# Optimization experiments

Hardware: AMD Instinct MI355X
Metric: run time of the kernel (lower is better)

## Reference

```python
import jax, jax.numpy as jnp
import numpy as np

E, H, KV, D = 2048, 32, 8, 64  # embed_dim, n_head, n_kv_head, head_dim
B, C = 1, 2048
G = H // KV  # GQA group size = 4


def setup_inputs() -> dict:
    key = jax.random.key(0)
    k0, k1, k2, k3, k4 = jax.random.split(key, 5)
    s = 0.02
    return {
        "x": jax.random.normal(k0, (B, C, E), dtype=jnp.float32),
        "W_q": jax.random.normal(k1, (H * D, E), dtype=jnp.float32) * s,
        "W_k": jax.random.normal(k2, (KV * D, E), dtype=jnp.float32) * s,
        "W_v": jax.random.normal(k3, (KV * D, E), dtype=jnp.float32) * s,
        "W_o": jax.random.normal(k4, (E, H * D), dtype=jnp.float32) * s,
    }


def reference(x, W_q, W_k, W_v, W_o):
    b, c, e = x.shape
    # bias-free projections (nn.Linear applies x @ W.T)
    Q = (x @ W_q.T).reshape(b, c, KV, G, D)   # [B,C,KV,G,D]
    K = (x @ W_k.T).reshape(b, c, KV, D)      # [B,C,KV,D]
    V = (x @ W_v.T).reshape(b, c, KV, D)
    scale = 1.0 / jnp.sqrt(jnp.float32(D))
    # grouped-query attention scores: query heads grouped per KV head
    scores = jnp.einsum("bqkgd,bskd->bkgqs", Q, K) * scale  # [B,KV,G,Cq,Cs]
    causal = jnp.tril(jnp.ones((c, c), dtype=bool))
    scores = jnp.where(causal, scores, jnp.finfo(scores.dtype).min)
    attn = jax.nn.softmax(scores, axis=-1)
    hidden = jnp.einsum("bkgqs,bskd->bqkgd", attn, V)  # [B,Cq,KV,G,D]
    hidden = hidden.reshape(b, c, H * D)
    return hidden @ W_o.T
```

## Files before the change

kernel.cpp:

```cpp
#include <hip/hip_runtime.h>
#include <stdint.h>
#include <stddef.h>

#define CLEN 2048
#define EMB  2048
#define NH   32
#define NKV  8
#define HD   64

#define SZ_X  (CLEN * EMB)
#define SZ_WQ (NH * HD * EMB)
#define SZ_WK (NKV * HD * EMB)
#define SZ_WV (NKV * HD * EMB)
#define SZ_WO (EMB * NH * HD)
#define SZ_ALL (SZ_X + SZ_WQ + SZ_WK + SZ_WV + SZ_WO)

typedef __attribute__((ext_vector_type(8))) short short8v;
typedef __attribute__((ext_vector_type(4))) short short4v;
typedef __attribute__((ext_vector_type(4))) float float4v;

#define MFMA16(A, B, C) __builtin_amdgcn_mfma_f32_16x16x32_bf16((A), (B), (C), 0, 0, 0)

__device__ __forceinline__ uint16_t f2bf(float f) {
  union { float f; unsigned int u; } c;
  c.f = f;
  return (uint16_t)((c.u + 0x7fffu + ((c.u >> 16) & 1u)) >> 16);
}

__device__ __forceinline__ void gload_lds16(const uint16_t* g, uint16_t* l) {
  __builtin_amdgcn_global_load_lds((const __attribute__((address_space(1))) void*)g,
                                   (__attribute__((address_space(3))) void*)l, 16, 0, 0);
}

__global__ __launch_bounds__(256) void cvt_all(
    const float* __restrict__ s0, const float* __restrict__ s1,
    const float* __restrict__ s2, const float* __restrict__ s3,
    const float* __restrict__ s4, uint16_t* __restrict__ dst)
{
  const long i = ((long)blockIdx.x * 256 + threadIdx.x) * 4;
  if (i >= SZ_ALL) return;
  const float* src;
  long off;
  if (i < SZ_X)                         { src = s0; off = i; }
  else if (i < SZ_X + SZ_WQ)            { src = s1; off = i - SZ_X; }
  else if (i < SZ_X + SZ_WQ + SZ_WK)    { src = s2; off = i - (SZ_X + SZ_WQ); }
  else if (i < SZ_X + SZ_WQ + SZ_WK + SZ_WV) { src = s3; off = i - (SZ_X + SZ_WQ + SZ_WK); }
  else                                  { src = s4; off = i - (SZ_X + SZ_WQ + SZ_WK + SZ_WV); }
  const float4v v = *(const float4v*)(src + off);
  short4v p;
#pragma unroll
  for (int j = 0; j < 4; ++j) p[j] = (short)f2bf(v[j]);
  *(short4v*)(dst + i) = p;
}

template <int NW, int OMODE>
__device__ __forceinline__ void gemm_bk64(
    const uint16_t* __restrict__ A, const uint16_t* __restrict__ B,
    uint16_t* __restrict__ Co, float* __restrict__ Cf,
    int m0, int n0, int M, int N, int Kd)
{
  __shared__ uint16_t As[128 * 64];
  __shared__ uint16_t Bs[32 * NW * 64];
  const int tid = threadIdx.x;
  const int w = tid >> 6, l = tid & 63;
  const int wr = (w >> 1) << 5;
  const int wc = (w & 1) * (NW << 4);
  const int lr = l & 15, lhi = l >> 4;
  const int swz = (lr & 7) << 4;

  float4v acc[2][NW] = {};

  const int sr8 = l >> 3;
  const int scol = (((l & 7) ^ sr8) << 3);

  for (int k0 = 0; k0 < Kd; k0 += 64) {
    __syncthreads();
    gload_lds16(A + (size_t)(m0 + (w << 3) + sr8) * Kd + k0 + scol,       As + w * 512);
    gload_lds16(A + (size_t)(m0 + ((w + 8) << 3) + sr8) * Kd + k0 + scol, As + (w + 8) * 512);
    gload_lds16(B + (size_t)(n0 + (w << 3) + sr8) * Kd + k0 + scol,       Bs + w * 512);
    if (NW == 4)
      gload_lds16(B + (size_t)(n0 + ((w + 8) << 3) + sr8) * Kd + k0 + scol, Bs + (w + 8) * 512);
    __syncthreads();

    short8v a[2][2], b[NW][2];
#pragma unroll
    for (int i = 0; i < 2; ++i) {
      const int row = wr + i * 16 + lr;
#pragma unroll
      for (int ks = 0; ks < 2; ++ks)
        a[i][ks] = *(const short8v*)((const char*)As + row * 128 + ((ks * 64 + lhi * 16) ^ swz));
    }
#pragma unroll
    for (int j = 0; j < NW; ++j) {
      const int row = wc + j * 16 + lr;
#pragma unroll
      for (int ks = 0; ks < 2; ++ks)
        b[j][ks] = *(const short8v*)((const char*)Bs + row * 128 + ((ks * 64 + lhi * 16) ^ swz));
    }
#pragma unroll
    for (int ks = 0; ks < 2; ++ks)
#pragma unroll
      for (int i = 0; i < 2; ++i)
#pragma unroll
        for (int j = 0; j < NW; ++j)
          acc[i][j] = MFMA16(a[i][ks], b[j][ks], acc[i][j]);
  }

  if (OMODE == 1) {
#pragma unroll
    for (int i = 0; i < 2; ++i) {
      const int m = m0 + wr + i * 16 + lhi * 4;
#pragma unroll
      for (int j = 0; j < NW; ++j) {
        const int n = n0 + wc + j * 16 + lr;
        short4v pk;
#pragma unroll
        for (int r = 0; r < 4; ++r) pk[r] = (short)f2bf(acc[i][j][r]);
        *(short4v*)(Co + (size_t)n * M + m) = pk;
      }
    }
  } else if (OMODE == 0) {
#pragma unroll
    for (int i = 0; i < 2; ++i) {
      const int m = m0 + wr + i * 16 + lhi * 4;
#pragma unroll
      for (int j = 0; j < NW; ++j) {
        const int n = n0 + wc + j * 16 + lr;
#pragma unroll
        for (int r = 0; r < 4; ++r)
          Co[(size_t)(m + r) * N + n] = f2bf(acc[i][j][r]);
      }
    }
  } else {
#pragma unroll
    for (int i = 0; i < 2; ++i) {
      const int m = m0 + wr + i * 16 + lhi * 4;
#pragma unroll
      for (int j = 0; j < NW; ++j) {
        const int n = n0 + wc + j * 16 + lr;
#pragma unroll
        for (int r = 0; r < 4; ++r)
          Cf[(size_t)(m + r) * N + n] = acc[i][j][r];
      }
    }
  }
}

__global__ __launch_bounds__(512) void qkv_gemm(
    const uint16_t* __restrict__ x,
    const uint16_t* __restrict__ Wq, const uint16_t* __restrict__ Wk,
    const uint16_t* __restrict__ Wv,
    uint16_t* __restrict__ Qw, uint16_t* __restrict__ Kw, uint16_t* __restrict__ Vtw)
{
  const int m0 = blockIdx.x << 7;
  const int bn = blockIdx.y;
  if (bn < 16) {
    gemm_bk64<4, 0>(x, Wq, Qw, nullptr, m0, bn << 7, CLEN, NH * HD, EMB);
  } else if (bn < 24) {
    gemm_bk64<2, 0>(x, Wk, Kw, nullptr, m0, (bn - 16) << 6, CLEN, NKV * HD, EMB);
  } else {
    gemm_bk64<2, 1>(x, Wv, Vtw, nullptr, m0, (bn - 24) << 6, CLEN, NKV * HD, EMB);
  }
}

__global__ __launch_bounds__(512) void out_gemm(
    const uint16_t* __restrict__ Hh, const uint16_t* __restrict__ Wo,
    float* __restrict__ out)
{
  gemm_bk64<2, 2>(Hh, Wo, nullptr, out, blockIdx.x << 7, blockIdx.y << 6, CLEN, EMB, NH * HD);
}

#define SCL 0.1803368801111244f

__global__ __launch_bounds__(256) void attn_fwd(
    const uint16_t* __restrict__ Q, const uint16_t* __restrict__ Kx,
    const uint16_t* __restrict__ Vt, uint16_t* __restrict__ Hd)
{
  const int h = blockIdx.y;
  const int x = blockIdx.x;
  const int kvh = h >> 2;
  const int tid = threadIdx.x, w = tid >> 6, l = tid & 63;
  const int lr = l & 15, lhi = l >> 4;

  __shared__ uint16_t Ks[2][64 * 64];
  __shared__ uint16_t Vs[2][64 * 64];
  __shared__ uint16_t Pl[4][16 * 72];

  short8v ones;
#pragma unroll
  for (int c = 0; c < 8; ++c) ones[c] = (short)0x3F80;

  const int sr8 = l >> 3;
  const int scol = (((l & 7) ^ sr8) << 3);

  for (int it = 0; it < 2; ++it) {
    const int qt = it ? (31 - x) : x;
    const int q0 = qt << 6;

    short8v qf0, qf1;
    {
      const uint16_t* qp = Q + (size_t)(q0 + w * 16 + lr) * (NH * HD) + h * HD + lhi * 8;
      qf0 = *(const short8v*)qp;
      qf1 = *(const short8v*)(qp + 32);
    }

    float4v o[4] = {};
    float4v osum = {};

    const int ntile = qt + 1;

#pragma unroll
    for (int i = 0; i < 2; ++i) {
      const int c = (i << 2) | w;
      const int srow = (c << 3) | sr8;
      gload_lds16(Kx + (size_t)srow * (NKV * HD) + kvh * HD + scol, Ks[0] + c * 512);
      gload_lds16(Vt + (size_t)(kvh * HD + srow) * CLEN + scol,     Vs[0] + c * 512);
    }
    __syncthreads();

    int cur = 0;
    for (int s = 0; s < ntile; ++s) {
      if (s + 1 < ntile) {
        const int kv1 = (s + 1) << 6;
#pragma unroll
        for (int i = 0; i < 2; ++i) {
          const int c = (i << 2) | w;
          const int srow = (c << 3) | sr8;
          gload_lds16(Kx + (size_t)(kv1 + srow) * (NKV * HD) + kvh * HD + scol,
                      Ks[cur ^ 1] + c * 512);
          gload_lds16(Vt + (size_t)(kvh * HD + srow) * CLEN + kv1 + scol,
                      Vs[cur ^ 1] + c * 512);
        }
      }

      const char* KsB = (const char*)Ks[cur];
      const char* VsB = (const char*)Vs[cur];

      float4v sf[4];
      __builtin_amdgcn_s_setprio(1);
#pragma unroll
      for (int nb = 0; nb < 4; ++nb) {
        const int row = nb * 16 + lr;
        const int rowb = row * 128, sw = (row & 7) << 4;
        float4v a0 = {};
        a0 = MFMA16(qf0, *(const short8v*)(KsB + ((rowb + lhi * 16) ^ sw)), a0);
        a0 = MFMA16(qf1, *(const short8v*)(KsB + ((rowb + 64 + lhi * 16) ^ sw)), a0);
        sf[nb] = a0;
      }
      __builtin_amdgcn_s_setprio(0);

      if (s == ntile - 1) {
        const int qbase = q0 + w * 16 + lhi * 4;
        const int kbase = (s << 6) + lr;
#pragma unroll
        for (int nb = 0; nb < 4; ++nb)
#pragma unroll
          for (int r = 0; r < 4; ++r) {
            float vv = sf[nb][r] * SCL;
            vv = (kbase + nb * 16 <= qbase + r) ? vv : -3e38f;
            sf[nb][r] = __builtin_amdgcn_exp2f(vv);
          }
      } else {
#pragma unroll
        for (int nb = 0; nb < 4; ++nb)
#pragma unroll
          for (int r = 0; r < 4; ++r)
            sf[nb][r] = __builtin_amdgcn_exp2f(sf[nb][r] * SCL);
      }

#pragma unroll
      for (int nb = 0; nb < 4; ++nb)
#pragma unroll
        for (int r = 0; r < 4; ++r)
          Pl[w][(lhi * 4 + r) * 72 + nb * 16 + lr] = f2bf(sf[nb][r]);
      const short8v pf0 = *(const short8v*)&Pl[w][lr * 72 + lhi * 8];
      const short8v pf1 = *(const short8v*)&Pl[w][lr * 72 + 32 + lhi * 8];

      __builtin_amdgcn_s_setprio(1);
#pragma unroll
      for (int j = 0; j < 4; ++j) {
        const int row = j * 16 + lr;
        const int rowb = row * 128, sw = (row & 7) << 4;
        o[j] = MFMA16(pf0, *(const short8v*)(VsB + ((rowb + lhi * 16) ^ sw)), o[j]);
        o[j] = MFMA16(pf1, *(const short8v*)(VsB + ((rowb + 64 + lhi * 16) ^ sw)), o[j]);
      }
      osum = MFMA16(pf0, ones, osum);
      osum = MFMA16(pf1, ones, osum);
      __builtin_amdgcn_s_setprio(0);

      __syncthreads();
      cur ^= 1;
    }

#pragma unroll
    for (int r = 0; r < 4; ++r) {
      const float inv = 1.0f / osum[r];
      const size_t qq = (size_t)(q0 + w * 16 + lhi * 4 + r);
#pragma unroll
      for (int j = 0; j < 4; ++j)
        Hd[qq * (NH * HD) + h * HD + j * 16 + lr] = f2bf(o[j][r] * inv);
    }
  }
}

extern "C" void kernel_launch(void* const* d_in, const int* in_sizes, int n_in,
                              void* d_out, int out_size, void* d_ws, size_t ws_size,
                              hipStream_t stream) {
  const float* x  = (const float*)d_in[0];
  const float* Wq = (const float*)d_in[1];
  const float* Wk = (const float*)d_in[2];
  const float* Wv = (const float*)d_in[3];
  const float* Wo = (const float*)d_in[4];

  uint16_t* ws  = (uint16_t*)d_ws;
  uint16_t* xb  = ws;
  uint16_t* Wqb = xb  + SZ_X;
  uint16_t* Wkb = Wqb + SZ_WQ;
  uint16_t* Wvb = Wkb + SZ_WK;
  uint16_t* Wob = Wvb + SZ_WV;
  uint16_t* Qw  = Wob + SZ_WO;
  uint16_t* Kw  = Qw  + (size_t)CLEN * (NH * HD);
  uint16_t* Vtw = Kw  + (size_t)CLEN * (NKV * HD);
  uint16_t* Hw  = Vtw + (size_t)CLEN * (NKV * HD);

  cvt_all<<<SZ_ALL / 1024, 256, 0, stream>>>(x, Wq, Wk, Wv, Wo, ws);
  qkv_gemm<<<dim3(16, 32), 512, 0, stream>>>(xb, Wqb, Wkb, Wvb, Qw, Kw, Vtw);
  attn_fwd<<<dim3(16, 32), 256, 0, stream>>>(Qw, Kw, Vtw, Hw);
  out_gemm<<<dim3(16, 32), 512, 0, stream>>>(Hw, Wob, (float*)d_out);
}
```

Before: 116.2 us.

## Process two KV tiles per attention iteration and fold softmax scale into Q

The attention loop now stages 128 KV rows per iteration, as two 64-row halves, in double-buffered LDS. It computes both QK^T blocks before the softmax and PV work, halving the number of barriers and giving more independent MFMA work to interleave. The softmax scale is applied in the Q projection epilogue, which removes a multiply per score, and P is rounded to bf16 with a cheaper round-half-up conversion. LDS use doubles, which may lower occupancy, and pre-scaling Q in bf16 slightly changes rounding.

```diff
diff --git a/kernel.cpp b/kernel.cpp
--- a/kernel.cpp
+++ b/kernel.cpp
@@ -21,10 +21,17 @@
 
 #define MFMA16(A, B, C) __builtin_amdgcn_mfma_f32_16x16x32_bf16((A), (B), (C), 0, 0, 0)
 
+#define SCL 0.1803368801111244f
+
 __device__ __forceinline__ uint16_t f2bf(float f) {
   union { float f; unsigned int u; } c;
   c.f = f;
   return (uint16_t)((c.u + 0x7fffu + ((c.u >> 16) & 1u)) >> 16);
+}
+__device__ __forceinline__ uint16_t f2bf_c(float f) {
+  union { float f; unsigned int u; } c;
+  c.f = f;
+  return (uint16_t)((c.u + 0x8000u) >> 16);
 }
 
 __device__ __forceinline__ void gload_lds16(const uint16_t* g, uint16_t* l) {
@@ -57,7 +64,7 @@
 __device__ __forceinline__ void gemm_bk64(
     const uint16_t* __restrict__ A, const uint16_t* __restrict__ B,
     uint16_t* __restrict__ Co, float* __restrict__ Cf,
-    int m0, int n0, int M, int N, int Kd)
+    int m0, int n0, int M, int N, int Kd, float oscale)
 {
   __shared__ uint16_t As[128 * 64];
   __shared__ uint16_t Bs[32 * NW * 64];
@@ -128,7 +135,7 @@
         const int n = n0 + wc + j * 16 + lr;
 #pragma unroll
         for (int r = 0; r < 4; ++r)
-          Co[(size_t)(m + r) * N + n] = f2bf(acc[i][j][r]);
+          Co[(size_t)(m + r) * N + n] = f2bf(acc[i][j][r] * oscale);
       }
     }
   } else {
@@ -155,11 +162,11 @@
   const int m0 = blockIdx.x << 7;
   const int bn = blockIdx.y;
   if (bn < 16) {
-    gemm_bk64<4, 0>(x, Wq, Qw, nullptr, m0, bn << 7, CLEN, NH * HD, EMB);
+    gemm_bk64<4, 0>(x, Wq, Qw, nullptr, m0, bn << 7, CLEN, NH * HD, EMB, SCL);
   } else if (bn < 24) {
-    gemm_bk64<2, 0>(x, Wk, Kw, nullptr, m0, (bn - 16) << 6, CLEN, NKV * HD, EMB);
+    gemm_bk64<2, 0>(x, Wk, Kw, nullptr, m0, (bn - 16) << 6, CLEN, NKV * HD, EMB, 1.0f);
   } else {
-    gemm_bk64<2, 1>(x, Wv, Vtw, nullptr, m0, (bn - 24) << 6, CLEN, NKV * HD, EMB);
+    gemm_bk64<2, 1>(x, Wv, Vtw, nullptr, m0, (bn - 24) << 6, CLEN, NKV * HD, EMB, 1.0f);
   }
 }
 
@@ -167,10 +174,8 @@
     const uint16_t* __restrict__ Hh, const uint16_t* __restrict__ Wo,
     float* __restrict__ out)
 {
-  gemm_bk64<2, 2>(Hh, Wo, nullptr, out, blockIdx.x << 7, blockIdx.y << 6, CLEN, EMB, NH * HD);
-}
-
-#define SCL 0.1803368801111244f
+  gemm_bk64<2, 2>(Hh, Wo, nullptr, out, blockIdx.x << 7, blockIdx.y << 6, CLEN, EMB, NH * HD, 1.0f);
+}
 
 __global__ __launch_bounds__(256) void attn_fwd(
     const uint16_t* __restrict__ Q, const uint16_t* __restrict__ Kx,
@@ -182,8 +187,8 @@
   const int tid = threadIdx.x, w = tid >> 6, l = tid & 63;
   const int lr = l & 15, lhi = l >> 4;
 
-  __shared__ uint16_t Ks[2][64 * 64];
-  __shared__ uint16_t Vs[2][64 * 64];
+  __shared__ uint16_t Ks[2][2][64 * 64];
+  __shared__ uint16_t Vs[2][2][64 * 64];
   __shared__ uint16_t Pl[4][16 * 72];
 
   short8v ones;
@@ -196,6 +201,7 @@
   for (int it = 0; it < 2; ++it) {
     const int qt = it ? (31 - x) : x;
     const int q0 = qt << 6;
+    const bool odd = (qt & 1) != 0;
 
     short8v qf0, qf1;
     {
@@ -207,57 +213,44 @@
     float4v o[4] = {};
     float4v osum = {};
 
-    const int ntile = qt + 1;
-
-#pragma unroll
-    for (int i = 0; i < 2; ++i) {
-      const int c = (i << 2) | w;
-      const int srow = (c << 3) | sr8;
-      gload_lds16(Kx + (size_t)srow * (NKV * HD) + kvh * HD + scol, Ks[0] + c * 512);
-      gload_lds16(Vt + (size_t)(kvh * HD + srow) * CLEN + scol,     Vs[0] + c * 512);
+    const int nd = (qt >> 1) + 1;
+
+#pragma unroll
+    for (int half = 0; half < 2; ++half) {
+      const int kb = half << 6;
+#pragma unroll
+      for (int i = 0; i < 2; ++i) {
+        const int c = (i << 2) | w;
+        const int srow = (c << 3) | sr8;
+        gload_lds16(Kx + (size_t)(kb + srow) * (NKV * HD) + kvh * HD + scol,
+                    Ks[0][half] + c * 512);
+        gload_lds16(Vt + (size_t)(kvh * HD + srow) * CLEN + kb + scol,
+                    Vs[0][half] + c * 512);
+      }
     }
     __syncthreads();
 
-    int cur = 0;
-    for (int s = 0; s < ntile; ++s) {
-      if (s + 1 < ntile) {
-        const int kv1 = (s + 1) << 6;
-#pragma unroll
-        for (int i = 0; i < 2; ++i) {
-          const int c = (i << 2) | w;
-          const int srow = (c << 3) | sr8;
-          gload_lds16(Kx + (size_t)(kv1 + srow) * (NKV * HD) + kvh * HD + scol,
-                      Ks[cur ^ 1] + c * 512);
-          gload_lds16(Vt + (size_t)(kvh * HD + srow) * CLEN + kv1 + scol,
-                      Vs[cur ^ 1] + c * 512);
-        }
-      }
-
-      const char* KsB = (const char*)Ks[cur];
-      const char* VsB = (const char*)Vs[cur];
-
-      float4v sf[4];
+    auto qk = [&](const uint16_t* KsB, float4v (&sf)[4]) {
       __builtin_amdgcn_s_setprio(1);
 #pragma unroll
       for (int nb = 0; nb < 4; ++nb) {
         const int row = nb * 16 + lr;
         const int rowb = row * 128, sw = (row & 7) << 4;
         float4v a0 = {};
-        a0 = MFMA16(qf0, *(const short8v*)(KsB + ((rowb + lhi * 16) ^ sw)), a0);
-        a0 = MFMA16(qf1, *(const short8v*)(KsB + ((rowb + 64 + lhi * 16) ^ sw)), a0);
+        a0 = MFMA16(qf0, *(const short8v*)((const char*)KsB + ((rowb + lhi * 16) ^ sw)), a0);
+        a0 = MFMA16(qf1, *(const short8v*)((const char*)KsB + ((rowb + 64 + lhi * 16) ^ sw)), a0);
         sf[nb] = a0;
       }
       __builtin_amdgcn_s_setprio(0);
-
-      if (s == ntile - 1) {
-        const int qbase = q0 + w * 16 + lhi * 4;
-        const int kbase = (s << 6) + lr;
+    };
+    auto smax = [&](float4v (&sf)[4], bool diag) {
+      if (diag) {
+        const int qb = w * 16 + lhi * 4;
 #pragma unroll
         for (int nb = 0; nb < 4; ++nb)
 #pragma unroll
           for (int r = 0; r < 4; ++r) {
-            float vv = sf[nb][r] * SCL;
-            vv = (kbase + nb * 16 <= qbase + r) ? vv : -3e38f;
+            const float vv = (nb * 16 + lr <= qb + r) ? sf[nb][r] : -3e38f;
             sf[nb][r] = __builtin_amdgcn_exp2f(vv);
           }
       } else {
@@ -265,28 +258,61 @@
         for (int nb = 0; nb < 4; ++nb)
 #pragma unroll
           for (int r = 0; r < 4; ++r)
-            sf[nb][r] = __builtin_amdgcn_exp2f(sf[nb][r] * SCL);
-      }
-
+            sf[nb][r] = __builtin_amdgcn_exp2f(sf[nb][r]);
+      }
+    };
+    auto pv = [&](const uint16_t* VsB, float4v (&sf)[4]) {
 #pragma unroll
       for (int nb = 0; nb < 4; ++nb)
 #pragma unroll
         for (int r = 0; r < 4; ++r)
-          Pl[w][(lhi * 4 + r) * 72 + nb * 16 + lr] = f2bf(sf[nb][r]);
+          Pl[w][(lhi * 4 + r) * 72 + nb * 16 + lr] = f2bf_c(sf[nb][r]);
       const short8v pf0 = *(const short8v*)&Pl[w][lr * 72 + lhi * 8];
       const short8v pf1 = *(const short8v*)&Pl[w][lr * 72 + 32 + lhi * 8];
-
       __builtin_amdgcn_s_setprio(1);
 #pragma unroll
       for (int j = 0; j < 4; ++j) {
         const int row = j * 16 + lr;
         const int rowb = row * 128, sw = (row & 7) << 4;
-        o[j] = MFMA16(pf0, *(const short8v*)(VsB + ((rowb + lhi * 16) ^ sw)), o[j]);
-        o[j] = MFMA16(pf1, *(const short8v*)(VsB + ((rowb + 64 + lhi * 16) ^ sw)), o[j]);
+        o[j] = MFMA16(pf0, *(const short8v*)((const char*)VsB + ((rowb + lhi * 16) ^ sw)), o[j]);
+        o[j] = MFMA16(pf1, *(const short8v*)((const char*)VsB + ((rowb + 64 + lhi * 16) ^ sw)), o[j]);
       }
       osum = MFMA16(pf0, ones, osum);
       osum = MFMA16(pf1, ones, osum);
       __builtin_amdgcn_s_setprio(0);
+    };
+
+    int cur = 0;
+    for (int s = 0; s < nd; ++s) {
+      if (s + 1 < nd) {
+        const int kv1 = (s + 1) << 7;
+#pragma unroll
+        for (int half = 0; half < 2; ++half) {
+          const int kb = kv1 + (half << 6);
+#pragma unroll
+          for (int i = 0; i < 2; ++i) {
+            const int c = (i << 2) | w;
+            const int srow = (c << 3) | sr8;
+            gload_lds16(Kx + (size_t)(kb + srow) * (NKV * HD) + kvh * HD + scol,
+                        Ks[cur ^ 1][half] + c * 512);
+            gload_lds16(Vt + (size_t)(kvh * HD + srow) * CLEN + kb + scol,
+                        Vs[cur ^ 1][half] + c * 512);
+          }
+        }
+      }
+
+      const bool last = (s == nd - 1);
+      const bool doB = !last || odd;
+
+      float4v sfA[4], sfB[4];
+      qk(Ks[cur][0], sfA);
+      if (doB) qk(Ks[cur][1], sfB);
+
+      smax(sfA, last && !odd);
+      if (doB) smax(sfB, last && odd);
+
+      pv(Vs[cur][0], sfA);
+      if (doB) pv(Vs[cur][1], sfB);
 
       __syncthreads();
       cur ^= 1;
```

Measured after the change: 112.5 us. 3.2% less time.

## Share K/V tiles across GQA group heads and fold softmax scale into Q

Applied to the files above, without the earlier changes.

The attention kernel now runs one 512-thread block per KV head and pair of 32-row query tiles. Its 8 waves cover the 4 query heads in the group, so each K/V tile loaded into LDS serves four heads instead of one. The softmax scale (log2e/sqrt(D)) is applied in the Q projection epilogue, which removes a multiply per score. P is also rounded to bf16 with a cheaper round-half-up conversion. The trade-off is fewer, larger blocks (256 instead of 512) with 32-row query tiles causally masked against 64-wide KV tiles, and an extra bf16 rounding of the scaled Q.

```diff
diff --git a/kernel.cpp b/kernel.cpp
--- a/kernel.cpp
+++ b/kernel.cpp
@@ -21,10 +21,17 @@
 
 #define MFMA16(A, B, C) __builtin_amdgcn_mfma_f32_16x16x32_bf16((A), (B), (C), 0, 0, 0)
 
+#define SCL 0.1803368801111244f
+
 __device__ __forceinline__ uint16_t f2bf(float f) {
   union { float f; unsigned int u; } c;
   c.f = f;
   return (uint16_t)((c.u + 0x7fffu + ((c.u >> 16) & 1u)) >> 16);
+}
+__device__ __forceinline__ uint16_t f2bf_c(float f) {
+  union { float f; unsigned int u; } c;
+  c.f = f;
+  return (uint16_t)((c.u + 0x8000u) >> 16);
 }
 
 __device__ __forceinline__ void gload_lds16(const uint16_t* g, uint16_t* l) {
@@ -57,7 +64,7 @@
 __device__ __forceinline__ void gemm_bk64(
     const uint16_t* __restrict__ A, const uint16_t* __restrict__ B,
     uint16_t* __restrict__ Co, float* __restrict__ Cf,
-    int m0, int n0, int M, int N, int Kd)
+    int m0, int n0, int M, int N, int Kd, float oscale)
 {
   __shared__ uint16_t As[128 * 64];
   __shared__ uint16_t Bs[32 * NW * 64];
@@ -128,7 +135,7 @@
         const int n = n0 + wc + j * 16 + lr;
 #pragma unroll
         for (int r = 0; r < 4; ++r)
-          Co[(size_t)(m + r) * N + n] = f2bf(acc[i][j][r]);
+          Co[(size_t)(m + r) * N + n] = f2bf(acc[i][j][r] * oscale);
       }
     }
   } else {
@@ -155,11 +162,11 @@
   const int m0 = blockIdx.x << 7;
   const int bn = blockIdx.y;
   if (bn < 16) {
-    gemm_bk64<4, 0>(x, Wq, Qw, nullptr, m0, bn << 7, CLEN, NH * HD, EMB);
+    gemm_bk64<4, 0>(x, Wq, Qw, nullptr, m0, bn << 7, CLEN, NH * HD, EMB, SCL);
   } else if (bn < 24) {
-    gemm_bk64<2, 0>(x, Wk, Kw, nullptr, m0, (bn - 16) << 6, CLEN, NKV * HD, EMB);
+    gemm_bk64<2, 0>(x, Wk, Kw, nullptr, m0, (bn - 16) << 6, CLEN, NKV * HD, EMB, 1.0f);
   } else {
-    gemm_bk64<2, 1>(x, Wv, Vtw, nullptr, m0, (bn - 24) << 6, CLEN, NKV * HD, EMB);
+    gemm_bk64<2, 1>(x, Wv, Vtw, nullptr, m0, (bn - 24) << 6, CLEN, NKV * HD, EMB, 1.0f);
   }
 }
 
@@ -167,24 +174,23 @@
     const uint16_t* __restrict__ Hh, const uint16_t* __restrict__ Wo,
     float* __restrict__ out)
 {
-  gemm_bk64<2, 2>(Hh, Wo, nullptr, out, blockIdx.x << 7, blockIdx.y << 6, CLEN, EMB, NH * HD);
-}
-
-#define SCL 0.1803368801111244f
-
-__global__ __launch_bounds__(256) void attn_fwd(
+  gemm_bk64<2, 2>(Hh, Wo, nullptr, out, blockIdx.x << 7, blockIdx.y << 6, CLEN, EMB, NH * HD, 1.0f);
+}
+
+__global__ __launch_bounds__(512) void attn_fwd(
     const uint16_t* __restrict__ Q, const uint16_t* __restrict__ Kx,
     const uint16_t* __restrict__ Vt, uint16_t* __restrict__ Hd)
 {
-  const int h = blockIdx.y;
-  const int x = blockIdx.x;
-  const int kvh = h >> 2;
+  const int kvh = blockIdx.y;
+  const int xp = blockIdx.x;
   const int tid = threadIdx.x, w = tid >> 6, l = tid & 63;
   const int lr = l & 15, lhi = l >> 4;
+  const int h = (kvh << 2) | (w >> 1);
+  const int wq = (w & 1) << 4;
 
   __shared__ uint16_t Ks[2][64 * 64];
   __shared__ uint16_t Vs[2][64 * 64];
-  __shared__ uint16_t Pl[4][16 * 72];
+  __shared__ uint16_t Pl[8][16 * 72];
 
   short8v ones;
 #pragma unroll
@@ -192,14 +198,17 @@
 
   const int sr8 = l >> 3;
   const int scol = (((l & 7) ^ sr8) << 3);
+  const int srow = (w << 3) | sr8;
 
   for (int it = 0; it < 2; ++it) {
-    const int qt = it ? (31 - x) : x;
-    const int q0 = qt << 6;
+    const int x = it ? (63 - xp) : xp;
+    const int q0 = x << 5;
+    const int qoff = (x & 1) << 5;
+    const int ntile = (x >> 1) + 1;
 
     short8v qf0, qf1;
     {
-      const uint16_t* qp = Q + (size_t)(q0 + w * 16 + lr) * (NH * HD) + h * HD + lhi * 8;
+      const uint16_t* qp = Q + (size_t)(q0 + wq + lr) * (NH * HD) + h * HD + lhi * 8;
       qf0 = *(const short8v*)qp;
       qf1 = *(const short8v*)(qp + 32);
     }
@@ -207,30 +216,18 @@
     float4v o[4] = {};
     float4v osum = {};
 
-    const int ntile = qt + 1;
-
-#pragma unroll
-    for (int i = 0; i < 2; ++i) {
-      const int c = (i << 2) | w;
-      const int srow = (c << 3) | sr8;
-      gload_lds16(Kx + (size_t)srow * (NKV * HD) + kvh * HD + scol, Ks[0] + c * 512);
-      gload_lds16(Vt + (size_t)(kvh * HD + srow) * CLEN + scol,     Vs[0] + c * 512);
-    }
+    gload_lds16(Kx + (size_t)srow * (NKV * HD) + kvh * HD + scol, Ks[0] + w * 512);
+    gload_lds16(Vt + (size_t)(kvh * HD + srow) * CLEN + scol,     Vs[0] + w * 512);
     __syncthreads();
 
     int cur = 0;
     for (int s = 0; s < ntile; ++s) {
       if (s + 1 < ntile) {
         const int kv1 = (s + 1) << 6;
-#pragma unroll
-        for (int i = 0; i < 2; ++i) {
-          const int c = (i << 2) | w;
-          const int srow = (c << 3) | sr8;
-          gload_lds16(Kx + (size_t)(kv1 + srow) * (NKV * HD) + kvh * HD + scol,
-                      Ks[cur ^ 1] + c * 512);
-          gload_lds16(Vt + (size_t)(kvh * HD + srow) * CLEN + kv1 + scol,
-                      Vs[cur ^ 1] + c * 512);
-        }
+        gload_lds16(Kx + (size_t)(kv1 + srow) * (NKV * HD) + kvh * HD + scol,
+                    Ks[cur ^ 1] + w * 512);
+        gload_lds16(Vt + (size_t)(kvh * HD + srow) * CLEN + kv1 + scol,
+                    Vs[cur ^ 1] + w * 512);
       }
 
       const char* KsB = (const char*)Ks[cur];
@@ -250,14 +247,12 @@
       __builtin_amdgcn_s_setprio(0);
 
       if (s == ntile - 1) {
-        const int qbase = q0 + w * 16 + lhi * 4;
-        const int kbase = (s << 6) + lr;
+        const int qb = qoff + wq + lhi * 4;
 #pragma unroll
         for (int nb = 0; nb < 4; ++nb)
 #pragma unroll
           for (int r = 0; r < 4; ++r) {
-            float vv = sf[nb][r] * SCL;
-            vv = (kbase + nb * 16 <= qbase + r) ? vv : -3e38f;
+            const float vv = (nb * 16 + lr <= qb + r) ? sf[nb][r] : -3e38f;
             sf[nb][r] = __builtin_amdgcn_exp2f(vv);
           }
       } else {
@@ -265,14 +260,14 @@
         for (int nb = 0; nb < 4; ++nb)
 #pragma unroll
           for (int r = 0; r < 4; ++r)
-            sf[nb][r] = __builtin_amdgcn_exp2f(sf[nb][r] * SCL);
+            sf[nb][r] = __builtin_amdgcn_exp2f(sf[nb][r]);
       }
 
 #pragma unroll
       for (int nb = 0; nb < 4; ++nb)
 #pragma unroll
         for (int r = 0; r < 4; ++r)
-          Pl[w][(lhi * 4 + r) * 72 + nb * 16 + lr] = f2bf(sf[nb][r]);
+          Pl[w][(lhi * 4 + r) * 72 + nb * 16 + lr] = f2bf_c(sf[nb][r]);
       const short8v pf0 = *(const short8v*)&Pl[w][lr * 72 + lhi * 8];
       const short8v pf1 = *(const short8v*)&Pl[w][lr * 72 + 32 + lhi * 8];
 
@@ -295,7 +290,7 @@
 #pragma unroll
     for (int r = 0; r < 4; ++r) {
       const float inv = 1.0f / osum[r];
-      const size_t qq = (size_t)(q0 + w * 16 + lhi * 4 + r);
+      const size_t qq = (size_t)(q0 + wq + lhi * 4 + r);
 #pragma unroll
       for (int j = 0; j < 4; ++j)
         Hd[qq * (NH * HD) + h * HD + j * 16 + lr] = f2bf(o[j][r] * inv);
@@ -325,6 +320,6 @@
 
   cvt_all<<<SZ_ALL / 1024, 256, 0, stream>>>(x, Wq, Wk, Wv, Wo, ws);
   qkv_gemm<<<dim3(16, 32), 512, 0, stream>>>(xb, Wqb, Wkb, Wvb, Qw, Kw, Vtw);
-  attn_fwd<<<dim3(16, 32), 256, 0, stream>>>(Qw, Kw, Vtw, Hw);
+  attn_fwd<<<dim3(32, 8), 512, 0, stream>>>(Qw, Kw, Vtw, Hw);
   out_gemm<<<dim3(16, 32), 512, 0, stream>>>(Hw, Wob, (float*)d_out);
 }
```

Measured after the change: 114.9 us, median of 4. No clear change (-1.1%).
